# Optimization experiments

Measured on AMD Instinct MI355X. Metric: run time of the kernel, lower is better.

## Reference

```python
import jax, jax.numpy as jnp
import numpy as np
from jax import lax

B, T, V, E, H, C, K = 256, 512, 50000, 128, 256, 128, 2


def setup_inputs() -> dict:
    key = jax.random.key(0)
    ks = jax.random.split(key, 16)
    s = lambda *sh: 1.0 / np.sqrt(sh[0])
    return {
        "input_current": jax.random.randint(ks[0], (B, T), 0, V, dtype=jnp.int32),
        "input_left": jax.random.randint(ks[1], (B, T), 0, V, dtype=jnp.int32),
        "input_right": jax.random.randint(ks[2], (B, T), 0, V, dtype=jnp.int32),
        "emb": jax.random.normal(ks[3], (V, E), jnp.float32) * 0.05,
        "Wf": jax.random.normal(ks[4], (E, H), jnp.float32) * s(E),
        "Uf": jax.random.normal(ks[5], (H, H), jnp.float32) * s(H),
        "bf": jnp.zeros((H,), jnp.float32),
        "Wb": jax.random.normal(ks[6], (E, H), jnp.float32) * s(E),
        "Ub": jax.random.normal(ks[7], (H, H), jnp.float32) * s(H),
        "bb": jnp.zeros((H,), jnp.float32),
        "Wc": jax.random.normal(ks[8], (2 * H + E, C), jnp.float32) * s(2 * H + E),
        "bc": jnp.zeros((C,), jnp.float32),
        "Wd": jax.random.normal(ks[9], (C, K), jnp.float32) * s(C),
        "bd": jnp.zeros((K,), jnp.float32),
    }


def _simple_rnn(x, W, U, b):
    # x: [B,T,E] -> outputs [B,T,H]; h_t = tanh(x_t W + b + h_{t-1} U)
    xw = jnp.einsum("bte,eh->bth", x, W) + b  # precompute input projection
    h0 = jnp.zeros((x.shape[0], U.shape[0]), x.dtype)

    def step(h, xw_t):
        h = jnp.tanh(xw_t + h @ U)
        return h, h

    _, hs = lax.scan(step, h0, jnp.swapaxes(xw, 0, 1))  # scan over time
    return jnp.swapaxes(hs, 0, 1)


def reference(input_current, input_left, input_right, emb, Wf, Uf, bf, Wb, Ub, bb, Wc, bc, Wd, bd):
    e_cur = emb[input_current]  # [B,T,E]
    e_left = emb[input_left]
    e_right = emb[input_right]
    x_left = _simple_rnn(e_left, Wf, Uf, bf)  # [B,T,H]
    # go_backwards RNN: process reversed sequence, then model reverses back
    x_right = _simple_rnn(e_right[:, ::-1], Wb, Ub, bb)[:, ::-1]  # [B,T,H]
    x = jnp.concatenate([x_left, e_cur, x_right], axis=2)  # [B,T,2H+E]
    x = jnp.tanh(jnp.einsum("btd,dc->btc", x, Wc) + bc)  # Conv1D k=1 + tanh
    x = jnp.max(x, axis=1)  # GlobalMaxPooling1D
    return jax.nn.sigmoid(x @ Wd + bd)  # [B,K]
```

## Files before the change

kernel.cpp:

```cpp
#include <hip/hip_runtime.h>
#include <hip/hip_bf16.h>


#define B_ 256
#define T_ 512
#define E_ 128
#define H_ 256
#define C_ 128

typedef __attribute__((ext_vector_type(8))) short short8;
typedef __attribute__((ext_vector_type(4))) float float4v;
typedef __attribute__((ext_vector_type(2))) unsigned int uint2v;

__device__ inline unsigned short f2bf(float f) {
  unsigned u = __float_as_uint(f);
  u += 0x7fffu + ((u >> 16) & 1u);
  return (unsigned short)(u >> 16);
}
__device__ inline unsigned pkbf(float a, float b) {
  __hip_bfloat162 h2 = __float22bfloat162_rn(float2{a, b});
  union { __hip_bfloat162 h; unsigned u; } cv;
  cv.h = h2;
  return cv.u;
}
__device__ inline float lo16f(unsigned u) { return __uint_as_float(u << 16); }
__device__ inline float hi16f(unsigned u) { return __uint_as_float(u & 0xffff0000u); }
__device__ inline float fast_tanh(float x) {
  float e = __expf(2.f * x);
  float r = __builtin_amdgcn_rcpf(e + 1.f);
  return __builtin_fmaf(-2.f, r, 1.f);
}
__device__ inline unsigned enc_f(float f) {
  unsigned u = __float_as_uint(f);
  return (u & 0x80000000u) ? ~u : (u | 0x80000000u);
}
__device__ inline float dec_f(unsigned key) {
  unsigned bits = (key & 0x80000000u) ? (key ^ 0x80000000u) : ~key;
  return __uint_as_float(bits);
}
__device__ inline void sync_lds() {
  asm volatile("s_waitcnt lgkmcnt(0)\n\ts_barrier" ::: "memory");
}

__device__ inline void st_agent(unsigned short* p, uint2v v) {
  union { uint2v v2; unsigned long long u; } cv;
  cv.v2 = v;
  __hip_atomic_store(reinterpret_cast<unsigned long long*>(p), cv.u,
                     __ATOMIC_RELAXED, __HIP_MEMORY_SCOPE_AGENT);
}

__device__ inline void wait_flag_ge(const int* f, int v) {
  if (__hip_atomic_load(f, __ATOMIC_RELAXED, __HIP_MEMORY_SCOPE_AGENT) < v) {
    while (__hip_atomic_load(f, __ATOMIC_RELAXED, __HIP_MEMORY_SCOPE_AGENT) <
           v)
      __builtin_amdgcn_s_sleep(8);
  }
  (void)__hip_atomic_load(f, __ATOMIC_ACQUIRE, __HIP_MEMORY_SCOPE_AGENT);
}

__global__ __launch_bounds__(256) void prep_kernel(
    const float* __restrict__ Wf, const float* __restrict__ Wb,
    const float* __restrict__ Wc, const float* __restrict__ Uf,
    const float* __restrict__ Ub,
    unsigned short* __restrict__ WfT, unsigned short* __restrict__ WbT,
    unsigned short* __restrict__ WcT, unsigned short* __restrict__ UfT,
    unsigned short* __restrict__ UbT, unsigned int* __restrict__ pooled,
    int* __restrict__ flags) {
  int gid = blockIdx.x * 256 + threadIdx.x;
  int stride = gridDim.x * 256;
  for (int i = gid; i < 128 * 256; i += stride) {
    int k = i >> 8, n = i & 255;
    WfT[n * 128 + k] = f2bf(Wf[i]);
    WbT[n * 128 + k] = f2bf(Wb[i]);
  }
  for (int i = gid; i < 640 * 128; i += stride) {
    int k = i >> 7, n = i & 127;
    WcT[n * 640 + k] = f2bf(Wc[i]);
  }
  for (int i = gid; i < 256 * 256; i += stride) {
    int k = i >> 8, n = i & 255;
    UfT[n * 256 + k] = f2bf(Uf[i]);
    UbT[n * 256 + k] = f2bf(Ub[i]);
  }
  for (int i = gid; i < B_ * C_; i += stride) pooled[i] = 0u;
  for (int i = gid; i < 1024; i += stride) flags[i] = 0;
}

__global__ __launch_bounds__(512, 1) void fused_kernel(
    const int* __restrict__ idxL, const int* __restrict__ idxR,
    const int* __restrict__ idxC, const float* __restrict__ emb,
    const unsigned short* __restrict__ WfT,
    const unsigned short* __restrict__ WbT,
    const float* __restrict__ bfv, const float* __restrict__ bbv,
    const unsigned short* __restrict__ UfT,
    const unsigned short* __restrict__ UbT,
    const unsigned short* __restrict__ WcT, const float* __restrict__ bc,
    unsigned short* x, unsigned int* __restrict__ pooled,
    int* __restrict__ flags) {
  const int blk = blockIdx.x;
  const int tid = threadIdx.x;
  const int lane = tid & 63, q = lane >> 4, l15 = lane & 15;

  __shared__ __attribute__((aligned(16))) unsigned short hbuf[2][16][280];

  if (blk < 32) {
    const int dir = blk & 1;
    const int btile = blk >> 1;
    const int b0 = btile * 16;
    const unsigned short* __restrict__ UT = dir ? UbT : UfT;
    const int xoff = dir ? 384 : 0;
    const int tstep = dir ? -1 : 1;
    const int t0 = dir ? (T_ - 1) : 0;
    const ptrdiff_t dstep = (ptrdiff_t)tstep * 640;
    const int wv = tid >> 6;
    int* fl = flags + (dir * 16 + btile) * 32;

    unsigned short* hb0 = &hbuf[0][0][0];
    unsigned short* hb1 = &hbuf[1][0][0];
    for (int i = tid; i < 16 * 280; i += 512) hb0[i] = 0;

    short8 ufr[2][8];
#pragma unroll
    for (int mt = 0; mt < 2; ++mt)
#pragma unroll
      for (int kt = 0; kt < 8; ++kt)
        ufr[mt][kt] = *(const short8*)(UT + (32 * wv + 16 * mt + l15) * H_ +
                                       kt * 32 + q * 8);

    int lastc = dir ? 31 : 0;
    wait_flag_ge(fl + lastc, 1);

    unsigned short* ptrS[2];
    const unsigned short* ptrL[2];
    uint2v curA[2], curB[2], infA[2], infB[2];
#pragma unroll
    for (int mt = 0; mt < 2; ++mt) {
      unsigned short* base =
          x + (size_t)(b0 + 2 * wv + mt) * T_ * 640 + xoff + lane * 4;
      unsigned short* bt = base + (ptrdiff_t)t0 * 640;
      curA[mt] = *(const uint2v*)(bt);
      curB[mt] = *(const uint2v*)(bt + dstep);
      infA[mt] = *(const uint2v*)(bt + 2 * dstep);
      infB[mt] = *(const uint2v*)(bt + 3 * dstep);
      ptrS[mt] = bt;
      ptrL[mt] = bt + 4 * dstep;
    }

    const unsigned lrd = l15 * 280;
    const unsigned lwr = l15 * 280 + 32 * wv;

    __syncthreads();

#pragma unroll 1
    for (int p = 0; p < 256; ++p) {
      int c = dir ? ((506 - 2 * p) >> 4) : ((2 * p + 5) >> 4);
      c = c < 0 ? 0 : (c > 31 ? 31 : c);
      if (c != lastc) {
        wait_flag_ge(fl + c, 1);
        lastc = c;
      }
      uint2v ldA[2], ldB[2];
      if (p < 254) {
#pragma unroll
        for (int mt = 0; mt < 2; ++mt) {
          ldA[mt] = *(const uint2v*)(ptrL[mt]);
          ldB[mt] = *(const uint2v*)(ptrL[mt] + dstep);
        }
      } else {
#pragma unroll
        for (int mt = 0; mt < 2; ++mt) {
          ldA[mt] = infA[mt];
          ldB[mt] = infB[mt];
        }
      }
#pragma unroll
      for (int mt = 0; mt < 2; ++mt) ptrL[mt] += 2 * dstep;

      {
        short8 afr[8];
#pragma unroll
        for (int kt = 0; kt < 8; ++kt)
          afr[kt] = *(const short8*)(hb0 + lrd + kt * 32 + q * 8);
        float4v acc[2];
#pragma unroll
        for (int mt = 0; mt < 2; ++mt)
          acc[mt] = (float4v){lo16f(curA[mt].x), hi16f(curA[mt].x),
                              lo16f(curA[mt].y), hi16f(curA[mt].y)};
#pragma unroll
        for (int kt = 0; kt < 8; ++kt)
#pragma unroll
          for (int mt = 0; mt < 2; ++mt)
            acc[mt] = __builtin_amdgcn_mfma_f32_16x16x32_bf16(
                ufr[mt][kt], afr[kt], acc[mt], 0, 0, 0);
#pragma unroll
        for (int mt = 0; mt < 2; ++mt) {
          uint2v hv = {pkbf(fast_tanh(acc[mt][0]), fast_tanh(acc[mt][1])),
                       pkbf(fast_tanh(acc[mt][2]), fast_tanh(acc[mt][3]))};
          *(uint2v*)(hb1 + lwr + 16 * mt + 4 * q) = hv;
          st_agent(ptrS[mt], hv);
        }
      }
      sync_lds();

      {
        short8 afr[8];
#pragma unroll
        for (int kt = 0; kt < 8; ++kt)
          afr[kt] = *(const short8*)(hb1 + lrd + kt * 32 + q * 8);
        float4v acc[2];
#pragma unroll
        for (int mt = 0; mt < 2; ++mt)
          acc[mt] = (float4v){lo16f(curB[mt].x), hi16f(curB[mt].x),
                              lo16f(curB[mt].y), hi16f(curB[mt].y)};
#pragma unroll
        for (int kt = 0; kt < 8; ++kt)
#pragma unroll
          for (int mt = 0; mt < 2; ++mt)
            acc[mt] = __builtin_amdgcn_mfma_f32_16x16x32_bf16(
                ufr[mt][kt], afr[kt], acc[mt], 0, 0, 0);
#pragma unroll
        for (int mt = 0; mt < 2; ++mt) {
          uint2v hv = {pkbf(fast_tanh(acc[mt][0]), fast_tanh(acc[mt][1])),
                       pkbf(fast_tanh(acc[mt][2]), fast_tanh(acc[mt][3]))};
          *(uint2v*)(hb0 + lwr + 16 * mt + 4 * q) = hv;
          st_agent(ptrS[mt] + dstep, hv);
        }
      }
#pragma unroll
      for (int mt = 0; mt < 2; ++mt) {
        ptrS[mt] += 2 * dstep;
        curA[mt] = infA[mt];
        curB[mt] = infB[mt];
        infA[mt] = ldA[mt];
        infB[mt] = ldB[mt];
      }
      if (((p + 1) & 7) == 0) {
        asm volatile("s_waitcnt vmcnt(0) lgkmcnt(0)\n\ts_barrier" ::: "memory");
        if (tid == 0) {
          const int cdone = dir ? (32 - ((p + 1) >> 3)) : (((p + 1) >> 3) - 1);
          __hip_atomic_store(fl + cdone, 2, __ATOMIC_RELAXED,
                             __HIP_MEMORY_SCOPE_AGENT);
        }
      } else {
        sync_lds();
      }
    }
    return;
  }

  if (blk < 1056) {
    const int b2 = blk - 32;
    const int z = b2 >> 5, r = b2 & 31;
    const int btile = r & 15, dirg = r >> 4;
    const int chunk = dirg ? (31 - z) : z;
    const int w8 = tid >> 6;
    const int g = w8 >> 2, wv = w8 & 3;
    const int t0 = chunk * 16 + g * 8;
    const int b0 = btile * 16;
    const int* __restrict__ idx = dirg ? idxR : idxL;
    const unsigned short* __restrict__ WT = dirg ? WbT : WfT;
    const float* __restrict__ bias = dirg ? bbv : bfv;

    short8 wfr[4][4];
#pragma unroll
    for (int mt = 0; mt < 4; ++mt)
#pragma unroll
      for (int kt = 0; kt < 4; ++kt)
        wfr[mt][kt] = *(const short8*)(WT + (64 * wv + 16 * mt + l15) * 128 +
                                       kt * 32 + q * 8);
    float4v bv[4];
#pragma unroll
    for (int mt = 0; mt < 4; ++mt)
      bv[mt] = *(const float4v*)(bias + 64 * wv + 16 * mt + 4 * q);

    int er[8];
#pragma unroll
    for (int j = 0; j < 8; ++j) er[j] = idx[(b0 + l15) * T_ + t0 + j];

    float4v g0[8];
#pragma unroll
    for (int kt = 0; kt < 4; ++kt) {
      const float* p8 = emb + (size_t)er[0] * E_ + kt * 32 + q * 8;
      g0[2 * kt] = *(const float4v*)p8;
      g0[2 * kt + 1] = *(const float4v*)(p8 + 4);
    }

#pragma unroll 1
    for (int j = 0; j < 8; ++j) {
      float4v gn[8];
      if (j < 7) {
#pragma unroll
        for (int kt = 0; kt < 4; ++kt) {
          const float* p8 = emb + (size_t)er[j + 1] * E_ + kt * 32 + q * 8;
          gn[2 * kt] = *(const float4v*)p8;
          gn[2 * kt + 1] = *(const float4v*)(p8 + 4);
        }
      }
      short8 efr[4];
#pragma unroll
      for (int kt = 0; kt < 4; ++kt) {
        union { unsigned u[4]; short8 s; } cv;
        cv.u[0] = pkbf(g0[2 * kt][0], g0[2 * kt][1]);
        cv.u[1] = pkbf(g0[2 * kt][2], g0[2 * kt][3]);
        cv.u[2] = pkbf(g0[2 * kt + 1][0], g0[2 * kt + 1][1]);
        cv.u[3] = pkbf(g0[2 * kt + 1][2], g0[2 * kt + 1][3]);
        efr[kt] = cv.s;
      }
      float4v acc[4];
#pragma unroll
      for (int mt = 0; mt < 4; ++mt) acc[mt] = (float4v){0.f, 0.f, 0.f, 0.f};
#pragma unroll
      for (int kt = 0; kt < 4; ++kt)
#pragma unroll
        for (int mt = 0; mt < 4; ++mt)
          acc[mt] = __builtin_amdgcn_mfma_f32_16x16x32_bf16(
              wfr[mt][kt], efr[kt], acc[mt], 0, 0, 0);
      const int t = t0 + j;
#pragma unroll
      for (int mt = 0; mt < 4; ++mt) {
        float4v v = acc[mt] + bv[mt];
        uint2v pk = {pkbf(v[0], v[1]), pkbf(v[2], v[3])};
        st_agent(x + ((size_t)(b0 + 4 * wv + mt) * T_ + t) * 640 +
                     dirg * 384 + lane * 4,
                 pk);
      }
      if (j < 7) {
#pragma unroll
        for (int kk = 0; kk < 8; ++kk) g0[kk] = gn[kk];
      }
    }
    __syncthreads();
    if (tid == 0) {
      __hip_atomic_store(flags + (dirg * 16 + btile) * 32 + chunk, 1,
                         __ATOMIC_RELAXED, __HIP_MEMORY_SCOPE_AGENT);
    }
    return;
  }

  {
    extern __shared__ unsigned short dtile[];
    const int b2 = blk - 1056;
    const int btile = b2 & 15, g = b2 >> 4;
    const int b0 = btile * 16;
    const int w = tid >> 6;

    short8 wfr[20];
#pragma unroll
    for (int kt = 0; kt < 20; ++kt)
      wfr[kt] =
          *(const short8*)(WcT + (size_t)(16 * w + l15) * 640 + kt * 32 + q * 8);
    float4v bv = *(const float4v*)(bc + 16 * w + 4 * q);

    float4v mx = (float4v){-1e30f, -1e30f, -1e30f, -1e30f};

    const int* flF = flags + btile * 32;
    const int* flB = flags + (16 + btile) * 32;

    const int srow = tid >> 4;
    const int tt0 = srow >> 4, row0 = srow & 15;
    const int ssub = tid & 15;
    const int f0 = 16 * (row0 & 7) + 8 * (row0 >> 3);

#pragma unroll 1
    for (int s = 0; s < 4; ++s) {
      const int rk = g + 8 * s;
      const int c = (rk & 1) ? (16 + (rk >> 1)) : (15 - (rk >> 1));
      wait_flag_ge(flF + c, 2);
      wait_flag_ge(flB + c, 2);
      const int t0c = c * 16;

      auto stage = [&](int jp, int buf) {
        const int t = t0c + 2 * jp + tt0;
        const unsigned short* src = x + ((size_t)(b0 + row0) * T_ + t) * 640;
        unsigned short* dst =
            dtile + (size_t)((buf * 2 + tt0) * 16 + row0) * 648;
        *(short8*)(dst + ssub * 8) = *(const short8*)(src + ssub * 8);
        *(short8*)(dst + 128 + ssub * 8) = *(const short8*)(src + 128 + ssub * 8);
        *(short8*)(dst + 384 + ssub * 8) = *(const short8*)(src + 384 + ssub * 8);
        *(short8*)(dst + 512 + ssub * 8) = *(const short8*)(src + 512 + ssub * 8);
        const int er = idxC[(b0 + ssub) * T_ + t];
        const float* ep = emb + (size_t)er * E_ + f0;
        float4v e0 = *(const float4v*)ep;
        float4v e1 = *(const float4v*)(ep + 4);
        *(uint2v*)(dst + 256 + 4 * ssub) =
            (uint2v){pkbf(e0[0], e0[1]), pkbf(e0[2], e0[3])};
        *(uint2v*)(dst + 320 + 4 * ssub) =
            (uint2v){pkbf(e1[0], e1[1]), pkbf(e1[2], e1[3])};
      };

      stage(0, 0);
      __syncthreads();
#pragma unroll 1
      for (int jp = 0; jp < 8; ++jp) {
        const int buf = jp & 1;
        if (jp < 7) stage(jp + 1, buf ^ 1);
        float4v acc0 = (float4v){0.f, 0.f, 0.f, 0.f};
        float4v acc1 = acc0;
#pragma unroll
        for (int kt = 0; kt < 20; ++kt) {
          int rrow, so1, so2;
          if (kt < 8) {
            rrow = 2 * kt + (q >> 1);
            so1 = 128 * (q & 1) + 4 * l15;
            so2 = so1 + 64;
          } else if (kt < 12) {
            rrow = 2 * (kt - 8) + (q >> 1) + 8 * (q & 1);
            so1 = 256 + 4 * l15;
            so2 = 320 + 4 * l15;
          } else {
            rrow = 2 * (kt - 12) + (q >> 1);
            so1 = 384 + 128 * (q & 1) + 4 * l15;
            so2 = so1 + 64;
          }
          const unsigned short* r0p =
              dtile + (size_t)((buf * 2) * 16 + rrow) * 648;
          const unsigned short* r1p = r0p + 16 * 648;
          uint2v a1 = *(const uint2v*)(r0p + so1);
          uint2v a2 = *(const uint2v*)(r0p + so2);
          uint2v b1 = *(const uint2v*)(r1p + so1);
          uint2v b2 = *(const uint2v*)(r1p + so2);
          union { unsigned u[4]; short8 s8; } cva, cvb;
          cva.u[0] = a1.x; cva.u[1] = a1.y; cva.u[2] = a2.x; cva.u[3] = a2.y;
          cvb.u[0] = b1.x; cvb.u[1] = b1.y; cvb.u[2] = b2.x; cvb.u[3] = b2.y;
          acc0 = __builtin_amdgcn_mfma_f32_16x16x32_bf16(wfr[kt], cva.s8,
                                                         acc0, 0, 0, 0);
          acc1 = __builtin_amdgcn_mfma_f32_16x16x32_bf16(wfr[kt], cvb.s8,
                                                         acc1, 0, 0, 0);
        }
#pragma unroll
        for (int i = 0; i < 4; ++i)
          mx[i] = fmaxf(fmaxf(mx[i], acc0[i]), acc1[i]);
        __syncthreads();
      }
    }
#pragma unroll
    for (int i = 0; i < 4; ++i)
      atomicMax(pooled + (b0 + l15) * C_ + 16 * w + 4 * q + i,
                enc_f(fast_tanh(mx[i] + bv[i])));
  }
}

__global__ __launch_bounds__(256) void dense_kernel(
    const unsigned int* __restrict__ pooled, const float* __restrict__ Wd,
    const float* __restrict__ bd, float* __restrict__ out) {
  int b = threadIdx.x;
  float s0 = bd[0], s1 = bd[1];
#pragma unroll 4
  for (int c = 0; c < C_; ++c) {
    float f = dec_f(pooled[b * C_ + c]);
    s0 += f * Wd[c * 2 + 0];
    s1 += f * Wd[c * 2 + 1];
  }
  out[b * 2 + 0] = 1.f / (1.f + __expf(-s0));
  out[b * 2 + 1] = 1.f / (1.f + __expf(-s1));
}

extern "C" void kernel_launch(void* const* d_in, const int* in_sizes, int n_in,
                              void* d_out, int out_size, void* d_ws, size_t ws_size,
                              hipStream_t stream) {
  const int* idxC = (const int*)d_in[0];
  const int* idxL = (const int*)d_in[1];
  const int* idxR = (const int*)d_in[2];
  const float* emb = (const float*)d_in[3];
  const float* Wf = (const float*)d_in[4];
  const float* Uf = (const float*)d_in[5];
  const float* bf_ = (const float*)d_in[6];
  const float* Wb = (const float*)d_in[7];
  const float* Ub = (const float*)d_in[8];
  const float* bb_ = (const float*)d_in[9];
  const float* Wc = (const float*)d_in[10];
  const float* bc = (const float*)d_in[11];
  const float* Wd = (const float*)d_in[12];
  const float* bd = (const float*)d_in[13];

  char* ws = (char*)d_ws;
  unsigned short* x = (unsigned short*)ws;
  unsigned int* pooled = (unsigned int*)(ws + 167772160);
  unsigned short* WfT = (unsigned short*)(ws + 167903232);
  unsigned short* WbT = WfT + 256 * 128;
  unsigned short* WcT = WbT + 256 * 128;
  unsigned short* UfT = WcT + 128 * 640;
  unsigned short* UbT = UfT + 256 * 256;
  int* flags = (int*)(ws + 168460288);

  prep_kernel<<<64, 256, 0, stream>>>(Wf, Wb, Wc, Uf, Ub, WfT, WbT, WcT, UfT,
                                      UbT, pooled, flags);
  fused_kernel<<<1184, 512, 120 * 1024, stream>>>(idxL, idxR, idxC, emb, WfT,
                                                  WbT, bf_, bb_, UfT, UbT, WcT,
                                                  bc, x, pooled, flags);
  dense_kernel<<<1, 256, 0, stream>>>(pooled, Wd, bd, (float*)d_out);
}
```

Baseline: 556.3 us.

## Merge forward and backward RNN recurrences into one block per batch tile

Each recurrence block now runs both directions, with the two halves of the block (256 threads each) handling forward and backward, and each wave owns 64 hidden units instead of 32. The recurrence grid shrinks from 32 to 16 blocks and the whole grid shrinks to match. Launch bounds move to 2 blocks per CU and dynamic shared memory is cut so two blocks can be resident, and the input prefetch depth drops from two steps ahead to one. The cost is twice the MFMA work per wave on the serial critical path, more register pressure under the tighter launch bound, barriers that now couple both directions, and less latency hiding from the shallower prefetch.

```diff
diff --git a/kernel.cpp b/kernel.cpp
--- a/kernel.cpp
+++ b/kernel.cpp
@@ -86,7 +86,7 @@
   for (int i = gid; i < 1024; i += stride) flags[i] = 0;
 }
 
-__global__ __launch_bounds__(512, 1) void fused_kernel(
+__global__ __launch_bounds__(512, 2) void fused_kernel(
     const int* __restrict__ idxL, const int* __restrict__ idxR,
     const int* __restrict__ idxC, const float* __restrict__ emb,
     const unsigned short* __restrict__ WfT,
@@ -101,99 +101,96 @@
   const int tid = threadIdx.x;
   const int lane = tid & 63, q = lane >> 4, l15 = lane & 15;
 
-  __shared__ __attribute__((aligned(16))) unsigned short hbuf[2][16][280];
-
-  if (blk < 32) {
-    const int dir = blk & 1;
-    const int btile = blk >> 1;
+  __shared__ __attribute__((aligned(16))) unsigned short hbuf[2][2][16][280];
+
+  if (blk < 16) {
+    const int dir = tid >> 8;
+    const int wv = (tid >> 6) & 3;
+    const int btile = blk;
     const int b0 = btile * 16;
     const unsigned short* __restrict__ UT = dir ? UbT : UfT;
     const int xoff = dir ? 384 : 0;
     const int tstep = dir ? -1 : 1;
     const int t0 = dir ? (T_ - 1) : 0;
     const ptrdiff_t dstep = (ptrdiff_t)tstep * 640;
-    const int wv = tid >> 6;
     int* fl = flags + (dir * 16 + btile) * 32;
 
-    unsigned short* hb0 = &hbuf[0][0][0];
-    unsigned short* hb1 = &hbuf[1][0][0];
-    for (int i = tid; i < 16 * 280; i += 512) hb0[i] = 0;
-
-    short8 ufr[2][8];
-#pragma unroll
-    for (int mt = 0; mt < 2; ++mt)
+    unsigned short* hb0 = &hbuf[dir][0][0][0];
+    unsigned short* hb1 = &hbuf[dir][1][0][0];
+    for (int i = tid; i < 2 * 2 * 16 * 280; i += 512) (&hbuf[0][0][0][0])[i] = 0;
+
+    short8 ufr[4][8];
+#pragma unroll
+    for (int mt = 0; mt < 4; ++mt)
 #pragma unroll
       for (int kt = 0; kt < 8; ++kt)
-        ufr[mt][kt] = *(const short8*)(UT + (32 * wv + 16 * mt + l15) * H_ +
+        ufr[mt][kt] = *(const short8*)(UT + (64 * wv + 16 * mt + l15) * H_ +
                                        kt * 32 + q * 8);
 
     int lastc = dir ? 31 : 0;
     wait_flag_ge(fl + lastc, 1);
 
-    unsigned short* ptrS[2];
-    const unsigned short* ptrL[2];
-    uint2v curA[2], curB[2], infA[2], infB[2];
-#pragma unroll
-    for (int mt = 0; mt < 2; ++mt) {
-      unsigned short* base =
-          x + (size_t)(b0 + 2 * wv + mt) * T_ * 640 + xoff + lane * 4;
-      unsigned short* bt = base + (ptrdiff_t)t0 * 640;
+    unsigned short* ptrS[4];
+    const unsigned short* ptrL[4];
+    uint2v curA[4], curB[4];
+#pragma unroll
+    for (int mt = 0; mt < 4; ++mt) {
+      unsigned short* bt = x + (size_t)(b0 + 4 * wv + mt) * T_ * 640 + xoff +
+                           lane * 4 + (ptrdiff_t)t0 * 640;
       curA[mt] = *(const uint2v*)(bt);
       curB[mt] = *(const uint2v*)(bt + dstep);
-      infA[mt] = *(const uint2v*)(bt + 2 * dstep);
-      infB[mt] = *(const uint2v*)(bt + 3 * dstep);
       ptrS[mt] = bt;
-      ptrL[mt] = bt + 4 * dstep;
+      ptrL[mt] = bt + 2 * dstep;
     }
 
     const unsigned lrd = l15 * 280;
-    const unsigned lwr = l15 * 280 + 32 * wv;
+    const unsigned lwr = l15 * 280 + 64 * wv;
 
     __syncthreads();
 
 #pragma unroll 1
     for (int p = 0; p < 256; ++p) {
-      int c = dir ? ((506 - 2 * p) >> 4) : ((2 * p + 5) >> 4);
+      int c = dir ? ((508 - 2 * p) >> 4) : ((2 * p + 3) >> 4);
       c = c < 0 ? 0 : (c > 31 ? 31 : c);
       if (c != lastc) {
         wait_flag_ge(fl + c, 1);
         lastc = c;
       }
-      uint2v ldA[2], ldB[2];
-      if (p < 254) {
-#pragma unroll
-        for (int mt = 0; mt < 2; ++mt) {
+      uint2v ldA[4], ldB[4];
+      if (p < 255) {
+#pragma unroll
+        for (int mt = 0; mt < 4; ++mt) {
           ldA[mt] = *(const uint2v*)(ptrL[mt]);
           ldB[mt] = *(const uint2v*)(ptrL[mt] + dstep);
         }
       } else {
 #pragma unroll
-        for (int mt = 0; mt < 2; ++mt) {
-          ldA[mt] = infA[mt];
-          ldB[mt] = infB[mt];
-        }
-      }
-#pragma unroll
-      for (int mt = 0; mt < 2; ++mt) ptrL[mt] += 2 * dstep;
+        for (int mt = 0; mt < 4; ++mt) {
+          ldA[mt] = curA[mt];
+          ldB[mt] = curB[mt];
+        }
+      }
+#pragma unroll
+      for (int mt = 0; mt < 4; ++mt) ptrL[mt] += 2 * dstep;
 
       {
         short8 afr[8];
 #pragma unroll
         for (int kt = 0; kt < 8; ++kt)
           afr[kt] = *(const short8*)(hb0 + lrd + kt * 32 + q * 8);
-        float4v acc[2];
-#pragma unroll
-        for (int mt = 0; mt < 2; ++mt)
+        float4v acc[4];
+#pragma unroll
+        for (int mt = 0; mt < 4; ++mt)
           acc[mt] = (float4v){lo16f(curA[mt].x), hi16f(curA[mt].x),
                               lo16f(curA[mt].y), hi16f(curA[mt].y)};
 #pragma unroll
         for (int kt = 0; kt < 8; ++kt)
 #pragma unroll
-          for (int mt = 0; mt < 2; ++mt)
+          for (int mt = 0; mt < 4; ++mt)
             acc[mt] = __builtin_amdgcn_mfma_f32_16x16x32_bf16(
                 ufr[mt][kt], afr[kt], acc[mt], 0, 0, 0);
 #pragma unroll
-        for (int mt = 0; mt < 2; ++mt) {
+        for (int mt = 0; mt < 4; ++mt) {
           uint2v hv = {pkbf(fast_tanh(acc[mt][0]), fast_tanh(acc[mt][1])),
                        pkbf(fast_tanh(acc[mt][2]), fast_tanh(acc[mt][3]))};
           *(uint2v*)(hb1 + lwr + 16 * mt + 4 * q) = hv;
@@ -207,19 +204,19 @@
 #pragma unroll
         for (int kt = 0; kt < 8; ++kt)
           afr[kt] = *(const short8*)(hb1 + lrd + kt * 32 + q * 8);
-        float4v acc[2];
-#pragma unroll
-        for (int mt = 0; mt < 2; ++mt)
+        float4v acc[4];
+#pragma unroll
+        for (int mt = 0; mt < 4; ++mt)
           acc[mt] = (float4v){lo16f(curB[mt].x), hi16f(curB[mt].x),
                               lo16f(curB[mt].y), hi16f(curB[mt].y)};
 #pragma unroll
         for (int kt = 0; kt < 8; ++kt)
 #pragma unroll
-          for (int mt = 0; mt < 2; ++mt)
+          for (int mt = 0; mt < 4; ++mt)
             acc[mt] = __builtin_amdgcn_mfma_f32_16x16x32_bf16(
                 ufr[mt][kt], afr[kt], acc[mt], 0, 0, 0);
 #pragma unroll
-        for (int mt = 0; mt < 2; ++mt) {
+        for (int mt = 0; mt < 4; ++mt) {
           uint2v hv = {pkbf(fast_tanh(acc[mt][0]), fast_tanh(acc[mt][1])),
                        pkbf(fast_tanh(acc[mt][2]), fast_tanh(acc[mt][3]))};
           *(uint2v*)(hb0 + lwr + 16 * mt + 4 * q) = hv;
@@ -227,16 +224,14 @@
         }
       }
 #pragma unroll
-      for (int mt = 0; mt < 2; ++mt) {
+      for (int mt = 0; mt < 4; ++mt) {
         ptrS[mt] += 2 * dstep;
-        curA[mt] = infA[mt];
-        curB[mt] = infB[mt];
-        infA[mt] = ldA[mt];
-        infB[mt] = ldB[mt];
+        curA[mt] = ldA[mt];
+        curB[mt] = ldB[mt];
       }
       if (((p + 1) & 7) == 0) {
         asm volatile("s_waitcnt vmcnt(0) lgkmcnt(0)\n\ts_barrier" ::: "memory");
-        if (tid == 0) {
+        if ((tid & 255) == 0) {
           const int cdone = dir ? (32 - ((p + 1) >> 3)) : (((p + 1) >> 3) - 1);
           __hip_atomic_store(fl + cdone, 2, __ATOMIC_RELAXED,
                              __HIP_MEMORY_SCOPE_AGENT);
@@ -248,8 +243,8 @@
     return;
   }
 
-  if (blk < 1056) {
-    const int b2 = blk - 32;
+  if (blk < 1040) {
+    const int b2 = blk - 16;
     const int z = b2 >> 5, r = b2 & 31;
     const int btile = r & 15, dirg = r >> 4;
     const int chunk = dirg ? (31 - z) : z;
@@ -339,7 +334,7 @@
 
   {
     extern __shared__ unsigned short dtile[];
-    const int b2 = blk - 1056;
+    const int b2 = blk - 1040;
     const int btile = b2 & 15, g = b2 >> 4;
     const int b0 = btile * 16;
     const int w = tid >> 6;
@@ -485,8 +480,8 @@
 
   prep_kernel<<<64, 256, 0, stream>>>(Wf, Wb, Wc, Uf, Ub, WfT, WbT, WcT, UfT,
                                       UbT, pooled, flags);
-  fused_kernel<<<1184, 512, 120 * 1024, stream>>>(idxL, idxR, idxC, emb, WfT,
-                                                  WbT, bf_, bb_, UfT, UbT, WcT,
-                                                  bc, x, pooled, flags);
+  fused_kernel<<<1168, 512, 82944, stream>>>(idxL, idxR, idxC, emb, WfT,
+                                             WbT, bf_, bb_, UfT, UbT, WcT,
+                                             bc, x, pooled, flags);
   dense_kernel<<<1, 256, 0, stream>>>(pooled, Wd, bd, (float*)d_out);
 }
```

Result: slower. 824.8 us (+48.3%).
